# Optimization experiments

Hardware: AMD Instinct MI355X
Metric: run time of the kernel (lower is better)

## Reference

```python
import jax, jax.numpy as jnp
import numpy as np

# OGB full_atom_feature_dims
FEAT_DIMS = np.array([119, 5, 12, 12, 10, 6, 6, 2, 2], dtype=np.int32)
OFFSETS = jnp.asarray(np.concatenate([[0], np.cumsum(FEAT_DIMS)[:-1]]), dtype=jnp.int32)  # [9]
TOTAL_ROWS = int(FEAT_DIMS.sum())  # 174
DIM = 256
N_CLASS = 10
B, MAX_NODE = 128, 1024


def setup_inputs() -> dict:
    key = jax.random.key(0)
    ks = jax.random.split(key, 16)
    # per-field valid categorical indices, stacked -> [B, MAX_NODE, 9]
    cols = [jax.random.randint(ks[i], (B, MAX_NODE), 0, int(FEAT_DIMS[i]), dtype=jnp.int32)
            for i in range(9)]
    node_feat = jnp.stack(cols, axis=-1)
    num_nodes = jax.random.randint(ks[9], (B,), 1, MAX_NODE + 1, dtype=jnp.int32)
    rxn_class = jax.random.randint(ks[10], (B,), 0, N_CLASS, dtype=jnp.int32)
    # learned params
    atom_emb = jax.random.normal(ks[11], (TOTAL_ROWS, DIM), dtype=jnp.float32) * 0.02
    rxn_emb = jax.random.normal(ks[12], (N_CLASS, DIM), dtype=jnp.float32) * 0.02
    lin_w = jax.random.normal(ks[13], (DIM, 2 * DIM), dtype=jnp.float32) * (1.0 / np.sqrt(2 * DIM))
    lin_b = jax.random.normal(ks[14], (DIM,), dtype=jnp.float32) * 0.01
    return {"node_feat": node_feat, "num_nodes": num_nodes, "rxn_class": rxn_class,
            "atom_emb": atom_emb, "rxn_emb": rxn_emb, "lin_w": lin_w, "lin_b": lin_b}


def reference(node_feat, num_nodes, rxn_class, atom_emb, rxn_emb, lin_w, lin_b):
    # AtomEncoder: sum of 9 per-field embedding lookups (tables concatenated with offsets)
    idx = node_feat + OFFSETS  # [B, N, 9]
    enc = atom_emb[idx].sum(axis=2)  # [B, N, dim]
    # zero-pad positions beyond num_nodes (ragged-to-dense scatter)
    mask = (jnp.arange(MAX_NODE)[None, :] < num_nodes[:, None])[..., None]  # [B, N, 1]
    enc = jnp.where(mask, enc, jnp.zeros((), dtype=enc.dtype))
    # class embedding broadcast over all node slots (including padding, as in original)
    cls = jnp.broadcast_to(rxn_emb[rxn_class][:, None, :], enc.shape)  # [B, N, dim]
    h = jnp.concatenate([enc, cls], axis=-1)  # [B, N, 2*dim]
    out = jnp.einsum('bnd,od->bno', h, lin_w) + lin_b  # [B, N, dim]
    return out
```

## Files before the change

### kernel.cpp

```cpp
#include <hip/hip_runtime.h>
#include <stdint.h>

#define BATCH 128
#define MAXN 1024
#define NF 9
#define DIM 256
#define NCLS 10

#define BASE1 119
#define BASE2 179
#define BASE3 299
#define QROWS 443

typedef __attribute__((ext_vector_type(4))) float f32x4;
typedef __attribute__((ext_vector_type(2))) uint32_t u32x2;

__device__ __forceinline__ ushort f32_to_bf16_rne(float x) {
  uint32_t u = __float_as_uint(x);
  u += 0x7fffu + ((u >> 16) & 1u);
  return (ushort)(u >> 16);
}

__device__ __forceinline__ f32x4 bf4_to_f32x4(u32x2 v) {
  f32x4 r;
  r.x = __uint_as_float(v.x << 16);
  r.y = __uint_as_float(v.x & 0xffff0000u);
  r.z = __uint_as_float(v.y << 16);
  r.w = __uint_as_float(v.y & 0xffff0000u);
  return r;
}

__global__ __launch_bounds__(256) void prep_kernel(
    const float* __restrict__ rxn_emb, const float* __restrict__ lin_w,
    const float* __restrict__ lin_b, const float* __restrict__ atom_emb,
    ushort* __restrict__ Qb, float* __restrict__ clsT)
{
  __shared__ float S[4][DIM];
  const int bid = blockIdx.x;
  const int t = threadIdx.x;
  const bool isCls = bid < 3;
  const int row0 = isCls ? bid * 4 : (bid - 3) * 4;
  const int rmax = isCls ? NCLS : QROWS;
  const int nrows = (rmax - row0 < 4) ? (rmax - row0) : 4;

#pragma unroll
  for (int r = 0; r < 4; ++r) {
    float v = 0.f;
    if (r < nrows) {
      const int q = row0 + r;
      if (isCls) {
        v = rxn_emb[q * DIM + t];
      } else if (q < BASE1) {
        v = atom_emb[q * DIM + t];
      } else if (q < BASE2) {
        int x = q - BASE1;
        v = atom_emb[(119 + x / 12) * DIM + t] + atom_emb[(124 + x % 12) * DIM + t];
      } else if (q < BASE3) {
        int x = q - BASE2;
        v = atom_emb[(136 + x / 10) * DIM + t] + atom_emb[(148 + x % 10) * DIM + t];
      } else {
        int x = q - BASE3;
        int i8 = x & 1, i7 = (x >> 1) & 1, y = x >> 2;
        v = atom_emb[(158 + y / 6) * DIM + t] + atom_emb[(164 + y % 6) * DIM + t]
          + atom_emb[(170 + i7) * DIM + t] + atom_emb[(172 + i8) * DIM + t];
      }
    }
    S[r][t] = v;
  }
  __syncthreads();

  const float* wrow = lin_w + (size_t)t * 2 * DIM + (isCls ? DIM : 0);
  const float init = isCls ? lin_b[t] : 0.f;
  float a0 = init, a1 = init, a2 = init, a3 = init;
#pragma unroll 4
  for (int d = 0; d < DIM; d += 4) {
    float4 w4 = *(const float4*)(wrow + d);
    a0 += w4.x * S[0][d] + w4.y * S[0][d + 1] + w4.z * S[0][d + 2] + w4.w * S[0][d + 3];
    a1 += w4.x * S[1][d] + w4.y * S[1][d + 1] + w4.z * S[1][d + 2] + w4.w * S[1][d + 3];
    a2 += w4.x * S[2][d] + w4.y * S[2][d + 1] + w4.z * S[2][d + 2] + w4.w * S[2][d + 3];
    a3 += w4.x * S[3][d] + w4.y * S[3][d + 1] + w4.z * S[3][d + 2] + w4.w * S[3][d + 3];
  }
  if (isCls) {
    if (0 < nrows) clsT[(row0 + 0) * DIM + t] = a0;
    if (1 < nrows) clsT[(row0 + 1) * DIM + t] = a1;
    if (2 < nrows) clsT[(row0 + 2) * DIM + t] = a2;
    if (3 < nrows) clsT[(row0 + 3) * DIM + t] = a3;
  } else {
    if (0 < nrows) Qb[(row0 + 0) * DIM + t] = f32_to_bf16_rne(a0);
    if (1 < nrows) Qb[(row0 + 1) * DIM + t] = f32_to_bf16_rne(a1);
    if (2 < nrows) Qb[(row0 + 2) * DIM + t] = f32_to_bf16_rne(a2);
    if (3 < nrows) Qb[(row0 + 3) * DIM + t] = f32_to_bf16_rne(a3);
  }
}

__global__ __launch_bounds__(256) void main_kernel(
    const int* __restrict__ node_feat, const int* __restrict__ num_nodes,
    const int* __restrict__ rxn_class,
    const ushort* __restrict__ Qb, const float* __restrict__ clsT,
    float* __restrict__ out)
{
  const int tid = threadIdx.x;
  const int lane = tid & 63;
  const int w = __builtin_amdgcn_readfirstlane(tid >> 6);
  const int wid = blockIdx.x * 4 + w;
  const int b = wid >> 7;
  const int n0 = (wid & 127) << 3;
  const int nn = num_nodes[b];

  const f32x4 cf = ((const f32x4*)clsT)[rxn_class[b] * 64 + lane];
  f32x4* __restrict__ outp = (f32x4*)out + ((size_t)(b * MAXN + n0)) * 64 + lane;

  if (n0 >= nn) {
#pragma unroll
    for (int i = 0; i < 8; ++i)
      __builtin_nontemporal_store(cf, outp + i * 64);
    return;
  }

  const int* __restrict__ p = node_feat + (size_t)(b * MAXN + n0) * NF;
  const u32x2* __restrict__ Q2 = (const u32x2*)Qb;

  if (n0 + 8 <= nn) {
#pragma unroll
    for (int i = 0; i < 8; ++i) {
      const int j0 = p[i * NF + 0];
      const int j1 = BASE1 + p[i * NF + 1] * 12 + p[i * NF + 2];
      const int j2 = BASE2 + p[i * NF + 3] * 10 + p[i * NF + 4];
      const int j3 = BASE3 + ((p[i * NF + 5] * 6 + p[i * NF + 6]) * 2 + p[i * NF + 7]) * 2 + p[i * NF + 8];
      const u32x2 v0 = Q2[j0 * 64 + lane];
      const u32x2 v1 = Q2[j1 * 64 + lane];
      const u32x2 v2 = Q2[j2 * 64 + lane];
      const u32x2 v3 = Q2[j3 * 64 + lane];
      const f32x4 s = (bf4_to_f32x4(v0) + bf4_to_f32x4(v1))
                    + (bf4_to_f32x4(v2) + bf4_to_f32x4(v3));
      __builtin_nontemporal_store(cf + s, outp + i * 64);
    }
    return;
  }

#pragma unroll
  for (int i = 0; i < 8; ++i) {
    const int j0 = p[i * NF + 0];
    const int j1 = BASE1 + p[i * NF + 1] * 12 + p[i * NF + 2];
    const int j2 = BASE2 + p[i * NF + 3] * 10 + p[i * NF + 4];
    const int j3 = BASE3 + ((p[i * NF + 5] * 6 + p[i * NF + 6]) * 2 + p[i * NF + 7]) * 2 + p[i * NF + 8];
    const u32x2 v0 = Q2[j0 * 64 + lane];
    const u32x2 v1 = Q2[j1 * 64 + lane];
    const u32x2 v2 = Q2[j2 * 64 + lane];
    const u32x2 v3 = Q2[j3 * 64 + lane];
    const float m = (n0 + i < nn) ? 1.f : 0.f;
    const f32x4 s = (bf4_to_f32x4(v0) + bf4_to_f32x4(v1))
                  + (bf4_to_f32x4(v2) + bf4_to_f32x4(v3));
    __builtin_nontemporal_store(cf + m * s, outp + i * 64);
  }
}

extern "C" void kernel_launch(void* const* d_in, const int* in_sizes, int n_in,
                              void* d_out, int out_size, void* d_ws, size_t ws_size,
                              hipStream_t stream) {
  const int* node_feat = (const int*)d_in[0];
  const int* num_nodes = (const int*)d_in[1];
  const int* rxn_class = (const int*)d_in[2];
  const float* atom_emb = (const float*)d_in[3];
  const float* rxn_emb = (const float*)d_in[4];
  const float* lin_w = (const float*)d_in[5];
  const float* lin_b = (const float*)d_in[6];
  float* outp = (float*)d_out;

  ushort* Qb = (ushort*)d_ws;
  float* clsT = (float*)((char*)d_ws + QROWS * DIM * sizeof(ushort));

  prep_kernel<<<3 + (QROWS + 3) / 4, 256, 0, stream>>>(rxn_emb, lin_w, lin_b,
                                                       atom_emb, Qb, clsT);
  main_kernel<<<4096, 256, 0, stream>>>(node_feat, num_nodes, rxn_class,
                                        Qb, clsT, outp);
}
```

Baseline: 44.69 us.

## Split table gathers across half-waves with 16-byte loads and cross-lane shuffle reduction

```diff
diff --git a/kernel.cpp b/kernel.cpp
--- a/kernel.cpp
+++ b/kernel.cpp
@@ -11,23 +11,14 @@
 #define BASE2 179
 #define BASE3 299
 #define QROWS 443
+#define TBLK 114
 
 typedef __attribute__((ext_vector_type(4))) float f32x4;
-typedef __attribute__((ext_vector_type(2))) uint32_t u32x2;
 
 __device__ __forceinline__ ushort f32_to_bf16_rne(float x) {
   uint32_t u = __float_as_uint(x);
   u += 0x7fffu + ((u >> 16) & 1u);
   return (ushort)(u >> 16);
-}
-
-__device__ __forceinline__ f32x4 bf4_to_f32x4(u32x2 v) {
-  f32x4 r;
-  r.x = __uint_as_float(v.x << 16);
-  r.y = __uint_as_float(v.x & 0xffff0000u);
-  r.z = __uint_as_float(v.y << 16);
-  r.w = __uint_as_float(v.y & 0xffff0000u);
-  return r;
 }
 
 __global__ __launch_bounds__(256) void prep_kernel(
@@ -107,51 +98,105 @@
   const int n0 = (wid & 127) << 3;
   const int nn = num_nodes[b];
 
-  const f32x4 cf = ((const f32x4*)clsT)[rxn_class[b] * 64 + lane];
-  f32x4* __restrict__ outp = (f32x4*)out + ((size_t)(b * MAXN + n0)) * 64 + lane;
+  const int li = lane & 31;
+  const int hi = lane >> 5;
+  const int slot = 2 * li + hi;
+
+  const f32x4 cf = ((const f32x4*)clsT)[rxn_class[b] * 64 + slot];
+  f32x4* __restrict__ outp = (f32x4*)out + ((size_t)(b * MAXN + n0)) * 64 + slot;
 
   if (n0 >= nn) {
 #pragma unroll
     for (int i = 0; i < 8; ++i)
-      __builtin_nontemporal_store(cf, outp + i * 64);
+      outp[i * 64] = cf;
     return;
   }
 
   const int* __restrict__ p = node_feat + (size_t)(b * MAXN + n0) * NF;
-  const u32x2* __restrict__ Q2 = (const u32x2*)Qb;
 
   if (n0 + 8 <= nn) {
+    int rAB[8], rCD[8];
 #pragma unroll
     for (int i = 0; i < 8; ++i) {
       const int j0 = p[i * NF + 0];
       const int j1 = BASE1 + p[i * NF + 1] * 12 + p[i * NF + 2];
       const int j2 = BASE2 + p[i * NF + 3] * 10 + p[i * NF + 4];
-      const int j3 = BASE3 + ((p[i * NF + 5] * 6 + p[i * NF + 6]) * 2 + p[i * NF + 7]) * 2 + p[i * NF + 8];
-      const u32x2 v0 = Q2[j0 * 64 + lane];
-      const u32x2 v1 = Q2[j1 * 64 + lane];
-      const u32x2 v2 = Q2[j2 * 64 + lane];
-      const u32x2 v3 = Q2[j3 * 64 + lane];
-      const f32x4 s = (bf4_to_f32x4(v0) + bf4_to_f32x4(v1))
-                    + (bf4_to_f32x4(v2) + bf4_to_f32x4(v3));
-      __builtin_nontemporal_store(cf + s, outp + i * 64);
+      const int j3 = BASE3 + ((p[i * NF + 5] * 6 + p[i * NF + 6]) * 2
+                              + p[i * NF + 7]) * 2 + p[i * NF + 8];
+      rAB[i] = hi ? j1 : j0;
+      rCD[i] = hi ? j3 : j2;
+    }
+
+    uint4 g[16];
+#pragma unroll
+    for (int i = 0; i < 8; ++i) {
+      const ushort* aAB = Qb + (size_t)rAB[i] * DIM + li * 8;
+      const ushort* aCD = Qb + (size_t)rCD[i] * DIM + li * 8;
+      asm volatile("global_load_dwordx4 %0, %1, off sc0"
+                   : "=v"(g[2 * i]) : "v"(aAB));
+      asm volatile("global_load_dwordx4 %0, %1, off sc0"
+                   : "=v"(g[2 * i + 1]) : "v"(aCD));
+    }
+
+    asm volatile("s_waitcnt vmcnt(0)" ::: "memory");
+    __builtin_amdgcn_sched_barrier(0);
+
+#pragma unroll
+    for (int i = 0; i < 8; ++i) {
+      const uint4 g1 = g[2 * i];
+      const uint4 g2 = g[2 * i + 1];
+      float pp[8];
+      pp[0] = __uint_as_float(g1.x << 16)        + __uint_as_float(g2.x << 16);
+      pp[1] = __uint_as_float(g1.x & 0xffff0000u) + __uint_as_float(g2.x & 0xffff0000u);
+      pp[2] = __uint_as_float(g1.y << 16)        + __uint_as_float(g2.y << 16);
+      pp[3] = __uint_as_float(g1.y & 0xffff0000u) + __uint_as_float(g2.y & 0xffff0000u);
+      pp[4] = __uint_as_float(g1.z << 16)        + __uint_as_float(g2.z << 16);
+      pp[5] = __uint_as_float(g1.z & 0xffff0000u) + __uint_as_float(g2.z & 0xffff0000u);
+      pp[6] = __uint_as_float(g1.w << 16)        + __uint_as_float(g2.w << 16);
+      pp[7] = __uint_as_float(g1.w & 0xffff0000u) + __uint_as_float(g2.w & 0xffff0000u);
+      f32x4 tot;
+#pragma unroll
+      for (int k = 0; k < 4; ++k) {
+        const float send = hi ? pp[k] : pp[4 + k];
+        const float own  = hi ? pp[4 + k] : pp[k];
+        const float recv = __shfl_xor(send, 32, 64);
+        tot[k] = cf[k] + own + recv;
+      }
+      outp[i * 64] = tot;
     }
     return;
   }
 
-#pragma unroll
+#pragma unroll 4
   for (int i = 0; i < 8; ++i) {
     const int j0 = p[i * NF + 0];
     const int j1 = BASE1 + p[i * NF + 1] * 12 + p[i * NF + 2];
     const int j2 = BASE2 + p[i * NF + 3] * 10 + p[i * NF + 4];
-    const int j3 = BASE3 + ((p[i * NF + 5] * 6 + p[i * NF + 6]) * 2 + p[i * NF + 7]) * 2 + p[i * NF + 8];
-    const u32x2 v0 = Q2[j0 * 64 + lane];
-    const u32x2 v1 = Q2[j1 * 64 + lane];
-    const u32x2 v2 = Q2[j2 * 64 + lane];
-    const u32x2 v3 = Q2[j3 * 64 + lane];
-    const float m = (n0 + i < nn) ? 1.f : 0.f;
-    const f32x4 s = (bf4_to_f32x4(v0) + bf4_to_f32x4(v1))
-                  + (bf4_to_f32x4(v2) + bf4_to_f32x4(v3));
-    __builtin_nontemporal_store(cf + m * s, outp + i * 64);
+    const int j3 = BASE3 + ((p[i * NF + 5] * 6 + p[i * NF + 6]) * 2
+                            + p[i * NF + 7]) * 2 + p[i * NF + 8];
+    const int rAB = hi ? j1 : j0;
+    const int rCD = hi ? j3 : j2;
+    const uint4 g1 = *(const uint4*)(Qb + (size_t)rAB * DIM + li * 8);
+    const uint4 g2 = *(const uint4*)(Qb + (size_t)rCD * DIM + li * 8);
+    float pp[8];
+    pp[0] = __uint_as_float(g1.x << 16)        + __uint_as_float(g2.x << 16);
+    pp[1] = __uint_as_float(g1.x & 0xffff0000u) + __uint_as_float(g2.x & 0xffff0000u);
+    pp[2] = __uint_as_float(g1.y << 16)        + __uint_as_float(g2.y << 16);
+    pp[3] = __uint_as_float(g1.y & 0xffff0000u) + __uint_as_float(g2.y & 0xffff0000u);
+    pp[4] = __uint_as_float(g1.z << 16)        + __uint_as_float(g2.z << 16);
+    pp[5] = __uint_as_float(g1.z & 0xffff0000u) + __uint_as_float(g2.z & 0xffff0000u);
+    pp[6] = __uint_as_float(g1.w << 16)        + __uint_as_float(g2.w << 16);
+    pp[7] = __uint_as_float(g1.w & 0xffff0000u) + __uint_as_float(g2.w & 0xffff0000u);
+    const float mval = (n0 + i < nn) ? 1.f : 0.f;
+    f32x4 tot;
+#pragma unroll
+    for (int k = 0; k < 4; ++k) {
+      const float send = hi ? pp[k] : pp[4 + k];
+      const float own  = hi ? pp[4 + k] : pp[k];
+      const float recv = __shfl_xor(send, 32, 64);
+      tot[k] = cf[k] + mval * (own + recv);
+    }
+    outp[i * 64] = tot;
   }
 }
 
@@ -170,8 +215,8 @@
   ushort* Qb = (ushort*)d_ws;
   float* clsT = (float*)((char*)d_ws + QROWS * DIM * sizeof(ushort));
 
-  prep_kernel<<<3 + (QROWS + 3) / 4, 256, 0, stream>>>(rxn_emb, lin_w, lin_b,
-                                                       atom_emb, Qb, clsT);
+  prep_kernel<<<TBLK, 256, 0, stream>>>(rxn_emb, lin_w, lin_b, atom_emb,
+                                        Qb, clsT);
   main_kernel<<<4096, 256, 0, stream>>>(node_feat, num_nodes, rxn_class,
                                         Qb, clsT, outp);
 }
```

After: 41.16 us. -7.9%, faster.
